# Kernel optimization log

Hardware: AMD Instinct MI355X
Metric: run time of the kernel (lower is better)

## Reference

```python
import jax, jax.numpy as jnp
import numpy as np

N2, N1, N0 = 16000, 4000, 1000   # leaf / mid / target node counts
DEG = 32                          # sampled neighbors per target
IN_DIM, OUT_DIM, H = 256, 64, 4
NEG = -9e15
ALPHA = 0.2                       # LeakyReLU slope


def setup_inputs() -> dict:
    key = jax.random.key(0)
    ks = jax.random.split(key, 10)
    s = 0.05  # xavier-ish scale
    x = jax.random.normal(ks[0], (N2, IN_DIM), jnp.float32)
    W0 = jax.random.normal(ks[1], (H, IN_DIM, OUT_DIM), jnp.float32) * s
    a0 = jax.random.normal(ks[2], (H, 2 * OUT_DIM), jnp.float32) * s
    W1 = jax.random.normal(ks[3], (H, OUT_DIM * H, OUT_DIM), jnp.float32) * s
    a1 = jax.random.normal(ks[4], (H, 2 * OUT_DIM), jnp.float32) * s
    lin_W = jax.random.normal(ks[5], (OUT_DIM * H, OUT_DIM * H), jnp.float32) * s
    lin_b = jax.random.normal(ks[6], (OUT_DIM * H,), jnp.float32) * s
    # level-1 edges: n1 targets, each with DEG sampled leaf neighbors + self-loop
    adj1_tgt = jnp.concatenate([jnp.repeat(jnp.arange(N1), DEG), jnp.arange(N1)]).astype(jnp.int32)
    adj1_nbr = jnp.concatenate([jax.random.randint(ks[7], (N1 * DEG,), 0, N2),
                                jnp.arange(N1)]).astype(jnp.int32)
    # level-0 edges: n0 targets, each with DEG sampled mid neighbors + self-loop
    adj0_tgt = jnp.concatenate([jnp.repeat(jnp.arange(N0), DEG), jnp.arange(N0)]).astype(jnp.int32)
    adj0_nbr = jnp.concatenate([jax.random.randint(ks[8], (N0 * DEG,), 0, N1),
                                jnp.arange(N0)]).astype(jnp.int32)
    return {"x": x, "W0": W0, "a0": a0, "W1": W1, "a1": a1,
            "lin_W": lin_W, "lin_b": lin_b,
            "adj1_tgt": adj1_tgt, "adj1_nbr": adj1_nbr,
            "adj0_tgt": adj0_tgt, "adj0_nbr": adj0_nbr,
            "n0": N0, "n1": N1}


def _att_layer(x, W, a, tgt, nbr, T):
    # x: [N, D], W: [H, D, O], a: [H, 2O]; multi-head GAT layer (eval mode, no dropout)
    h = jnp.einsum('nd,hdo->hno', x, W)                      # [H, N, O]
    O = h.shape[-1]
    e = jax.nn.leaky_relu(
        jnp.einsum('heo,ho->he', h[:, tgt], a[:, :O]) +
        jnp.einsum('heo,ho->he', h[:, nbr], a[:, O:]), ALPHA)  # [H, E]
    N = h.shape[1]
    att = jnp.full((h.shape[0], T, N), NEG, x.dtype).at[:, tgt, nbr].set(e)
    att = jax.nn.softmax(att, axis=-1)                        # dense edge-softmax
    hp = jax.nn.elu(jnp.einsum('htn,hno->hto', att, h))       # [H, T, O]
    return jnp.transpose(hp, (1, 0, 2)).reshape(T, -1)        # cat heads -> [T, H*O]


def reference(x, W0, a0, W1, a1, lin_W, lin_b,
              adj1_tgt, adj1_nbr, adj0_tgt, adj0_nbr, n0, n1):
    x1 = _att_layer(x, W0, a0, adj1_tgt, adj1_nbr, n1)   # [n1, H*O]
    x2 = _att_layer(x1, W1, a1, adj0_tgt, adj0_nbr, n0)  # [n0, H*O]
    return jnp.tanh(x2 @ lin_W.T + lin_b)                # Linear + Tanh
```

## Files before the change

### kernel.cpp

```cpp
#include <hip/hip_runtime.h>
#include <math.h>

#define N2C 16000
#define N1C 4000
#define N0C 1000
#define DEG 32
#define CH 256
#define NHEAD 4
#define ODIM 64
#define ALPHA 0.2f
#define LDP 264

typedef __attribute__((ext_vector_type(8))) short bf16x8;
typedef __attribute__((ext_vector_type(4))) float f32x4;

__device__ __forceinline__ ushort f2bf(float f) {
    unsigned u = __float_as_uint(f);
    unsigned r = (u + 0x7fffu + ((u >> 16) & 1u)) >> 16;
    return (ushort)r;
}
__device__ __forceinline__ float bf2f(ushort h) {
    return __uint_as_float(((unsigned)h) << 16);
}

__global__ __launch_bounds__(256) void repack_kernel(
    const float* __restrict__ W0, const float* __restrict__ W1,
    const float* __restrict__ linW,
    ushort* __restrict__ Wth, ushort* __restrict__ Wtl)
{
    int g = blockIdx.x * 256 + threadIdx.x;
    int mat = g >> 16;
    int idx = g & 65535;
    int c = idx >> 8, k = idx & 255;
    float v;
    if (mat == 0)      v = W0[(c >> 6) * (256 * 64) + k * 64 + (c & 63)];
    else if (mat == 1) v = W1[(c >> 6) * (256 * 64) + k * 64 + (c & 63)];
    else               v = linW[c * 256 + k];
    ushort h = f2bf(v);
    Wth[g] = h;
    Wtl[g] = f2bf(v - bf2f(h));
}

template<int RT, int EPI, int AF32, int SC>
__global__ __launch_bounds__(256) void gemm_mfma(
    const float* __restrict__ Af,
    const ushort* __restrict__ Ah, const ushort* __restrict__ Al,
    const ushort* __restrict__ Bh, const ushort* __restrict__ Bl,
    const float* __restrict__ bias, const float* __restrict__ avec,
    float* __restrict__ out, float* __restrict__ s_t, float* __restrict__ s_n, int M)
{
    __shared__ ushort sah[AF32 ? RT * 16 * LDP : 1];
    __shared__ ushort sal[AF32 ? RT * 16 * LDP : 1];

    const int wave = threadIdx.x >> 6;
    const int lane = threadIdx.x & 63;
    const int quad = lane >> 4, l16 = lane & 15;
    const int row0 = blockIdx.x * (RT * 16);
    const int col0 = wave * 64;

    if (AF32) {
        for (int idx = threadIdx.x; idx < RT * 16 * 64; idx += 256) {
            int row = idx >> 6, c4 = idx & 63;
            int gr = row0 + row; if (gr >= M) gr = M - 1;
            float4 f = ((const float4*)Af)[gr * 64 + c4];
            ushort4 h, l;
            h.x = f2bf(f.x); l.x = f2bf(f.x - bf2f(h.x));
            h.y = f2bf(f.y); l.y = f2bf(f.y - bf2f(h.y));
            h.z = f2bf(f.z); l.z = f2bf(f.z - bf2f(h.z));
            h.w = f2bf(f.w); l.w = f2bf(f.w - bf2f(h.w));
            *(ushort4*)(&sah[row * LDP + c4 * 4]) = h;
            *(ushort4*)(&sal[row * LDP + c4 * 4]) = l;
        }
        __syncthreads();
    }

    f32x4 acc[RT][4];
#pragma unroll
    for (int r = 0; r < RT; ++r)
#pragma unroll
        for (int c = 0; c < 4; ++c) acc[r][c] = (f32x4){0.f, 0.f, 0.f, 0.f};

    int arow[RT];
#pragma unroll
    for (int r = 0; r < RT; ++r) {
        int rr = row0 + r * 16 + l16;
        arow[r] = (rr < M) ? rr : (M - 1);
    }
    const int kbase = quad * 8;

    for (int k0 = 0; k0 < 256; k0 += 32) {
        bf16x8 a_h[RT], a_l[RT], b_h[4], b_l[4];
#pragma unroll
        for (int r = 0; r < RT; ++r) {
            if (AF32) {
                int loff = (r * 16 + l16) * LDP + k0 + kbase;
                a_h[r] = *(const bf16x8*)(&sah[loff]);
                a_l[r] = *(const bf16x8*)(&sal[loff]);
            } else {
                int off = arow[r] * 256 + k0 + kbase;
                a_h[r] = *(const bf16x8*)(Ah + off);
                a_l[r] = *(const bf16x8*)(Al + off);
            }
        }
#pragma unroll
        for (int c = 0; c < 4; ++c) {
            int off = (col0 + c * 16 + l16) * 256 + k0 + kbase;
            b_h[c] = *(const bf16x8*)(Bh + off);
            b_l[c] = *(const bf16x8*)(Bl + off);
        }
#pragma unroll
        for (int r = 0; r < RT; ++r)
#pragma unroll
            for (int c = 0; c < 4; ++c) {
                acc[r][c] = __builtin_amdgcn_mfma_f32_16x16x32_bf16(a_h[r], b_h[c], acc[r][c], 0, 0, 0);
                acc[r][c] = __builtin_amdgcn_mfma_f32_16x16x32_bf16(a_h[r], b_l[c], acc[r][c], 0, 0, 0);
                acc[r][c] = __builtin_amdgcn_mfma_f32_16x16x32_bf16(a_l[r], b_h[c], acc[r][c], 0, 0, 0);
            }
    }

#pragma unroll
    for (int r = 0; r < RT; ++r)
#pragma unroll
        for (int c = 0; c < 4; ++c) {
            int col = col0 + c * 16 + l16;
#pragma unroll
            for (int reg = 0; reg < 4; ++reg) {
                int row = row0 + r * 16 + quad * 4 + reg;
                if (row < M) {
                    float v = acc[r][c][reg];
                    if (EPI == 1) v = tanhf(v + bias[col]);
                    out[row * 256 + col] = v;
                }
            }
        }

    if (SC) {
        float at[4], an[4];
#pragma unroll
        for (int c = 0; c < 4; ++c) {
            at[c] = avec[wave * 128 + c * 16 + l16];
            an[c] = avec[wave * 128 + 64 + c * 16 + l16];
        }
#pragma unroll
        for (int r = 0; r < RT; ++r) {
            float pt[4] = {0.f, 0.f, 0.f, 0.f}, pn[4] = {0.f, 0.f, 0.f, 0.f};
#pragma unroll
            for (int c = 0; c < 4; ++c)
#pragma unroll
                for (int reg = 0; reg < 4; ++reg) {
                    pt[reg] += acc[r][c][reg] * at[c];
                    pn[reg] += acc[r][c][reg] * an[c];
                }
#pragma unroll
            for (int reg = 0; reg < 4; ++reg)
#pragma unroll
                for (int m = 1; m < 16; m <<= 1) {
                    pt[reg] += __shfl_xor(pt[reg], m);
                    pn[reg] += __shfl_xor(pn[reg], m);
                }
            if (l16 == 0) {
#pragma unroll
                for (int reg = 0; reg < 4; ++reg) {
                    int row = row0 + r * 16 + quad * 4 + reg;
                    if (row < M) {
                        s_t[wave * M + row] = pt[reg];
                        s_n[wave * M + row] = pn[reg];
                    }
                }
            }
        }
    }
}

__global__ __launch_bounds__(256) void att_kernel(
    const float* __restrict__ hprev, const int* __restrict__ nbr_arr,
    const float* __restrict__ s_t, const float* __restrict__ s_n,
    ushort* __restrict__ outhi, ushort* __restrict__ outlo, int T, int Nsrc)
{
    __shared__ int nbr[DEG + 1];
    __shared__ float att_s[NHEAD][DEG + 3];
    __shared__ float4 red[4][64];
    const int tgt = blockIdx.x;
    const int t = threadIdx.x;
    const int lane = t & 63;
    if (t < DEG) nbr[t] = nbr_arr[tgt * DEG + t];
    else if (t == DEG) nbr[DEG] = nbr_arr[T * DEG + tgt];
    __syncthreads();

    {
        const int hd = t >> 6;
        int me = (lane <= DEG) ? nbr[lane] : -1;
        int k = (lane <= DEG) ? 1 : 0;
#pragma unroll
        for (int j = 0; j < DEG; ++j) {
            int v = __shfl(me, j);
            if (j < lane && v == me) k = 0;
        }
        float e = s_t[hd * Nsrc + tgt] + ((lane <= DEG) ? s_n[hd * Nsrc + me] : 0.f);
        e = (e >= 0.f) ? e : ALPHA * e;
        float em = k ? e : -1e30f;
        float m = em;
#pragma unroll
        for (int off = 1; off < 64; off <<= 1) m = fmaxf(m, __shfl_xor(m, off));
        float w = k ? __expf(e - m) : 0.f;
        float Z = w;
#pragma unroll
        for (int off = 1; off < 64; off <<= 1) Z += __shfl_xor(Z, off);
        if (lane <= DEG) att_s[hd][lane] = w / Z;
    }
    __syncthreads();

    const int cq = t & 63;
    const int rg = t >> 6;
    const int hd = cq >> 4;
    const float4* hp4 = (const float4*)hprev;
    float4 acc = make_float4(0.f, 0.f, 0.f, 0.f);
#pragma unroll
    for (int ii = 0; ii < 9; ++ii) {
        int i = rg + ii * 4;
        if (i <= DEG) {
            float w = att_s[hd][i];
            float4 v = hp4[(size_t)nbr[i] * 64 + cq];
            acc.x += w * v.x; acc.y += w * v.y;
            acc.z += w * v.z; acc.w += w * v.w;
        }
    }
    red[rg][cq] = acc;
    __syncthreads();
    if (t < 64) {
        float4 s0 = red[0][t], s1 = red[1][t], s2 = red[2][t], s3 = red[3][t];
        float4 s;
        s.x = s0.x + s1.x + s2.x + s3.x;
        s.y = s0.y + s1.y + s2.y + s3.y;
        s.z = s0.z + s1.z + s2.z + s3.z;
        s.w = s0.w + s1.w + s2.w + s3.w;
        s.x = (s.x > 0.f) ? s.x : expm1f(s.x);
        s.y = (s.y > 0.f) ? s.y : expm1f(s.y);
        s.z = (s.z > 0.f) ? s.z : expm1f(s.z);
        s.w = (s.w > 0.f) ? s.w : expm1f(s.w);
        ushort4 h, l;
        h.x = f2bf(s.x); l.x = f2bf(s.x - bf2f(h.x));
        h.y = f2bf(s.y); l.y = f2bf(s.y - bf2f(h.y));
        h.z = f2bf(s.z); l.z = f2bf(s.z - bf2f(h.z));
        h.w = f2bf(s.w); l.w = f2bf(s.w - bf2f(h.w));
        ((ushort4*)outhi)[tgt * 64 + t] = h;
        ((ushort4*)outlo)[tgt * 64 + t] = l;
    }
}

extern "C" void kernel_launch(void* const* d_in, const int* in_sizes, int n_in,
                              void* d_out, int out_size, void* d_ws, size_t ws_size,
                              hipStream_t stream)
{
    const float* x    = (const float*)d_in[0];
    const float* W0   = (const float*)d_in[1];
    const float* a0   = (const float*)d_in[2];
    const float* W1   = (const float*)d_in[3];
    const float* a1   = (const float*)d_in[4];
    const float* linW = (const float*)d_in[5];
    const float* linb = (const float*)d_in[6];
    const int* adj1_nbr = (const int*)d_in[8];
    const int* adj0_nbr = (const int*)d_in[10];

    char* base = (char*)d_ws;
    ushort* Wth = (ushort*)base;
    ushort* Wtl = Wth + 3 * 65536;
    float*  st  = (float*)(base + 786432);
    float*  sn  = st + 65536;
    float*  h0  = (float*)(base + 1310720);
    ushort* xhi = (ushort*)(base + 1310720 + 16384000);
    ushort* xlo = xhi + 4096000;

    repack_kernel<<<768, 256, 0, stream>>>(W0, W1, linW, Wth, Wtl);

    gemm_mfma<2, 0, 1, 1><<<N2C / 32, 256, 0, stream>>>(
        x, nullptr, nullptr, Wth, Wtl, nullptr, a0, h0, st, sn, N2C);
    att_kernel<<<N1C, 256, 0, stream>>>(h0, adj1_nbr, st, sn, xhi, xlo, N1C, N2C);

    gemm_mfma<1, 0, 0, 1><<<N1C / 16, 256, 0, stream>>>(
        nullptr, xhi, xlo, Wth + 65536, Wtl + 65536, nullptr, a1, h0, st, sn, N1C);
    att_kernel<<<N0C, 256, 0, stream>>>(h0, adj0_nbr, st, sn, xhi, xlo, N0C, N1C);

    gemm_mfma<1, 1, 0, 0><<<(N0C + 15) / 16, 256, 0, stream>>>(
        nullptr, xhi, xlo, Wth + 131072, Wtl + 131072, linb, nullptr,
        (float*)d_out, nullptr, nullptr, N0C);
}
```

Measured before the change: 166.8 us.

## Fuse attention aggregation into the following GEMM via shared-memory staging

Attention softmax and neighbor aggregation now run inside the next layer's GEMM kernel. Each block computes 16 target rows, one per wave per iteration, and writes the split bf16 hi/lo results into shared memory. The GEMM tile then reads A from LDS instead of global memory. This removes two kernel launches and the global round-trip of the intermediate bf16 activations, but the aggregation kernels drop from 4000/1000 blocks to 250/63, so less parallelism is available for the gather-bound part.

```diff
diff --git a/kernel.cpp b/kernel.cpp
--- a/kernel.cpp
+++ b/kernel.cpp
@@ -5,9 +5,7 @@
 #define N1C 4000
 #define N0C 1000
 #define DEG 32
-#define CH 256
 #define NHEAD 4
-#define ODIM 64
 #define ALPHA 0.2f
 #define LDP 264
 
@@ -41,24 +39,21 @@
     Wtl[g] = f2bf(v - bf2f(h));
 }
 
-template<int RT, int EPI, int AF32, int SC>
-__global__ __launch_bounds__(256) void gemm_mfma(
+template<int RT, int EPI, int AMODE, int SC>
+__device__ __forceinline__ void gemm_tile(
+    int row0, int M,
     const float* __restrict__ Af,
-    const ushort* __restrict__ Ah, const ushort* __restrict__ Al,
     const ushort* __restrict__ Bh, const ushort* __restrict__ Bl,
     const float* __restrict__ bias, const float* __restrict__ avec,
-    float* __restrict__ out, float* __restrict__ s_t, float* __restrict__ s_n, int M)
-{
-    __shared__ ushort sah[AF32 ? RT * 16 * LDP : 1];
-    __shared__ ushort sal[AF32 ? RT * 16 * LDP : 1];
-
+    float* __restrict__ out, float* __restrict__ s_t, float* __restrict__ s_n,
+    ushort* sah, ushort* sal)
+{
     const int wave = threadIdx.x >> 6;
     const int lane = threadIdx.x & 63;
     const int quad = lane >> 4, l16 = lane & 15;
-    const int row0 = blockIdx.x * (RT * 16);
     const int col0 = wave * 64;
 
-    if (AF32) {
+    if (AMODE == 1) {
         for (int idx = threadIdx.x; idx < RT * 16 * 64; idx += 256) {
             int row = idx >> 6, c4 = idx & 63;
             int gr = row0 + row; if (gr >= M) gr = M - 1;
@@ -80,27 +75,14 @@
 #pragma unroll
         for (int c = 0; c < 4; ++c) acc[r][c] = (f32x4){0.f, 0.f, 0.f, 0.f};
 
-    int arow[RT];
-#pragma unroll
-    for (int r = 0; r < RT; ++r) {
-        int rr = row0 + r * 16 + l16;
-        arow[r] = (rr < M) ? rr : (M - 1);
-    }
     const int kbase = quad * 8;
-
     for (int k0 = 0; k0 < 256; k0 += 32) {
         bf16x8 a_h[RT], a_l[RT], b_h[4], b_l[4];
 #pragma unroll
         for (int r = 0; r < RT; ++r) {
-            if (AF32) {
-                int loff = (r * 16 + l16) * LDP + k0 + kbase;
-                a_h[r] = *(const bf16x8*)(&sah[loff]);
-                a_l[r] = *(const bf16x8*)(&sal[loff]);
-            } else {
-                int off = arow[r] * 256 + k0 + kbase;
-                a_h[r] = *(const bf16x8*)(Ah + off);
-                a_l[r] = *(const bf16x8*)(Al + off);
-            }
+            int loff = (r * 16 + l16) * LDP + k0 + kbase;
+            a_h[r] = *(const bf16x8*)(&sah[loff]);
+            a_l[r] = *(const bf16x8*)(&sal[loff]);
         }
 #pragma unroll
         for (int c = 0; c < 4; ++c) {
@@ -172,80 +154,93 @@
     }
 }
 
-__global__ __launch_bounds__(256) void att_kernel(
+__global__ __launch_bounds__(256) void gemm1_kernel(
+    const float* __restrict__ x, const float* __restrict__ a0,
+    const ushort* __restrict__ Bh, const ushort* __restrict__ Bl,
+    float* __restrict__ h0, float* __restrict__ s_t, float* __restrict__ s_n)
+{
+    __shared__ ushort sah[32 * LDP];
+    __shared__ ushort sal[32 * LDP];
+    gemm_tile<2, 0, 1, 1>(blockIdx.x * 32, N2C, x, Bh, Bl, nullptr, a0,
+                          h0, s_t, s_n, sah, sal);
+}
+
+template<int EPI, int SC>
+__global__ __launch_bounds__(256) void ag_kernel(
     const float* __restrict__ hprev, const int* __restrict__ nbr_arr,
-    const float* __restrict__ s_t, const float* __restrict__ s_n,
-    ushort* __restrict__ outhi, ushort* __restrict__ outlo, int T, int Nsrc)
-{
-    __shared__ int nbr[DEG + 1];
-    __shared__ float att_s[NHEAD][DEG + 3];
-    __shared__ float4 red[4][64];
-    const int tgt = blockIdx.x;
-    const int t = threadIdx.x;
-    const int lane = t & 63;
-    if (t < DEG) nbr[t] = nbr_arr[tgt * DEG + t];
-    else if (t == DEG) nbr[DEG] = nbr_arr[T * DEG + tgt];
+    const float* __restrict__ s_tin, const float* __restrict__ s_nin,
+    const ushort* __restrict__ Bh, const ushort* __restrict__ Bl,
+    const float* __restrict__ bias, const float* __restrict__ avec,
+    float* __restrict__ out, float* __restrict__ s_tout, float* __restrict__ s_nout,
+    int T, int Nsrc)
+{
+    __shared__ ushort sah[16 * LDP];
+    __shared__ ushort sal[16 * LDP];
+    __shared__ float wts[4][NHEAD][DEG + 2];
+
+    const int wave = threadIdx.x >> 6;
+    const int lane = threadIdx.x & 63;
+    const int row0 = blockIdx.x * 16;
+    const float4* hp4 = (const float4*)hprev;
+
+#pragma unroll
+    for (int r = 0; r < 4; ++r) {
+        const int tg = r * 4 + wave;
+        const int tgt = row0 + tg;
+        if (tgt < T) {
+            int me = 0;
+            if (lane < DEG) me = nbr_arr[tgt * DEG + lane];
+            else if (lane == DEG) me = nbr_arr[T * DEG + tgt];
+            int k = (lane <= DEG) ? 1 : 0;
+#pragma unroll
+            for (int j = 0; j < DEG; ++j) {
+                int v = __shfl(me, j);
+                if (j < lane && v == me) k = 0;
+            }
+#pragma unroll
+            for (int hd = 0; hd < NHEAD; ++hd) {
+                float e = s_tin[hd * Nsrc + tgt] + s_nin[hd * Nsrc + me];
+                e = (e >= 0.f) ? e : ALPHA * e;
+                float em = k ? e : -1e30f;
+                float m = em;
+#pragma unroll
+                for (int off = 1; off < 64; off <<= 1) m = fmaxf(m, __shfl_xor(m, off));
+                float w = k ? __expf(e - m) : 0.f;
+                float Z = w;
+#pragma unroll
+                for (int off = 1; off < 64; off <<= 1) Z += __shfl_xor(Z, off);
+                if (lane <= DEG) wts[wave][hd][lane] = w / Z;
+            }
+            const int hd = lane >> 4;
+            float4 acc = make_float4(0.f, 0.f, 0.f, 0.f);
+#pragma unroll
+            for (int e = 0; e <= DEG; ++e) {
+                int row = __shfl(me, e);
+                float wt = wts[wave][hd][e];
+                float4 v = hp4[(size_t)row * 64 + lane];
+                acc.x += wt * v.x; acc.y += wt * v.y;
+                acc.z += wt * v.z; acc.w += wt * v.w;
+            }
+            acc.x = (acc.x > 0.f) ? acc.x : expm1f(acc.x);
+            acc.y = (acc.y > 0.f) ? acc.y : expm1f(acc.y);
+            acc.z = (acc.z > 0.f) ? acc.z : expm1f(acc.z);
+            acc.w = (acc.w > 0.f) ? acc.w : expm1f(acc.w);
+            ushort4 h, l;
+            h.x = f2bf(acc.x); l.x = f2bf(acc.x - bf2f(h.x));
+            h.y = f2bf(acc.y); l.y = f2bf(acc.y - bf2f(h.y));
+            h.z = f2bf(acc.z); l.z = f2bf(acc.z - bf2f(h.z));
+            h.w = f2bf(acc.w); l.w = f2bf(acc.w - bf2f(h.w));
+            *(ushort4*)(&sah[tg * LDP + lane * 4]) = h;
+            *(ushort4*)(&sal[tg * LDP + lane * 4]) = l;
+        } else {
+            ushort4 z = make_ushort4(0, 0, 0, 0);
+            *(ushort4*)(&sah[tg * LDP + lane * 4]) = z;
+            *(ushort4*)(&sal[tg * LDP + lane * 4]) = z;
+        }
+    }
     __syncthreads();
-
-    {
-        const int hd = t >> 6;
-        int me = (lane <= DEG) ? nbr[lane] : -1;
-        int k = (lane <= DEG) ? 1 : 0;
-#pragma unroll
-        for (int j = 0; j < DEG; ++j) {
-            int v = __shfl(me, j);
-            if (j < lane && v == me) k = 0;
-        }
-        float e = s_t[hd * Nsrc + tgt] + ((lane <= DEG) ? s_n[hd * Nsrc + me] : 0.f);
-        e = (e >= 0.f) ? e : ALPHA * e;
-        float em = k ? e : -1e30f;
-        float m = em;
-#pragma unroll
-        for (int off = 1; off < 64; off <<= 1) m = fmaxf(m, __shfl_xor(m, off));
-        float w = k ? __expf(e - m) : 0.f;
-        float Z = w;
-#pragma unroll
-        for (int off = 1; off < 64; off <<= 1) Z += __shfl_xor(Z, off);
-        if (lane <= DEG) att_s[hd][lane] = w / Z;
-    }
-    __syncthreads();
-
-    const int cq = t & 63;
-    const int rg = t >> 6;
-    const int hd = cq >> 4;
-    const float4* hp4 = (const float4*)hprev;
-    float4 acc = make_float4(0.f, 0.f, 0.f, 0.f);
-#pragma unroll
-    for (int ii = 0; ii < 9; ++ii) {
-        int i = rg + ii * 4;
-        if (i <= DEG) {
-            float w = att_s[hd][i];
-            float4 v = hp4[(size_t)nbr[i] * 64 + cq];
-            acc.x += w * v.x; acc.y += w * v.y;
-            acc.z += w * v.z; acc.w += w * v.w;
-        }
-    }
-    red[rg][cq] = acc;
-    __syncthreads();
-    if (t < 64) {
-        float4 s0 = red[0][t], s1 = red[1][t], s2 = red[2][t], s3 = red[3][t];
-        float4 s;
-        s.x = s0.x + s1.x + s2.x + s3.x;
-        s.y = s0.y + s1.y + s2.y + s3.y;
-        s.z = s0.z + s1.z + s2.z + s3.z;
-        s.w = s0.w + s1.w + s2.w + s3.w;
-        s.x = (s.x > 0.f) ? s.x : expm1f(s.x);
-        s.y = (s.y > 0.f) ? s.y : expm1f(s.y);
-        s.z = (s.z > 0.f) ? s.z : expm1f(s.z);
-        s.w = (s.w > 0.f) ? s.w : expm1f(s.w);
-        ushort4 h, l;
-        h.x = f2bf(s.x); l.x = f2bf(s.x - bf2f(h.x));
-        h.y = f2bf(s.y); l.y = f2bf(s.y - bf2f(h.y));
-        h.z = f2bf(s.z); l.z = f2bf(s.z - bf2f(h.z));
-        h.w = f2bf(s.w); l.w = f2bf(s.w - bf2f(h.w));
-        ((ushort4*)outhi)[tgt * 64 + t] = h;
-        ((ushort4*)outlo)[tgt * 64 + t] = l;
-    }
+    gemm_tile<1, EPI, 2, SC>(row0, T, nullptr, Bh, Bl, bias, avec,
+                             out, s_tout, s_nout, sah, sal);
 }
 
 extern "C" void kernel_launch(void* const* d_in, const int* in_sizes, int n_in,
@@ -261,27 +256,26 @@
     const float* linb = (const float*)d_in[6];
     const int* adj1_nbr = (const int*)d_in[8];
     const int* adj0_nbr = (const int*)d_in[10];
-
-    char* base = (char*)d_ws;
-    ushort* Wth = (ushort*)base;
-    ushort* Wtl = Wth + 3 * 65536;
-    float*  st  = (float*)(base + 786432);
-    float*  sn  = st + 65536;
-    float*  h0  = (float*)(base + 1310720);
-    ushort* xhi = (ushort*)(base + 1310720 + 16384000);
-    ushort* xlo = xhi + 4096000;
+    char* ws = (char*)d_ws;
+
+    ushort* Wth = (ushort*)ws;
+    ushort* Wtl = (ushort*)(ws + 393216);
+    float*  st0 = (float*)(ws + 786432);
+    float*  sn0 = (float*)(ws + 1048576);
+    float*  st1 = (float*)(ws + 1310720);
+    float*  sn1 = (float*)(ws + 1376256);
+    float*  h0  = (float*)(ws + 1441792);
+    float*  h1  = (float*)(ws + 17825792);
 
     repack_kernel<<<768, 256, 0, stream>>>(W0, W1, linW, Wth, Wtl);
 
-    gemm_mfma<2, 0, 1, 1><<<N2C / 32, 256, 0, stream>>>(
-        x, nullptr, nullptr, Wth, Wtl, nullptr, a0, h0, st, sn, N2C);
-    att_kernel<<<N1C, 256, 0, stream>>>(h0, adj1_nbr, st, sn, xhi, xlo, N1C, N2C);
-
-    gemm_mfma<1, 0, 0, 1><<<N1C / 16, 256, 0, stream>>>(
-        nullptr, xhi, xlo, Wth + 65536, Wtl + 65536, nullptr, a1, h0, st, sn, N1C);
-    att_kernel<<<N0C, 256, 0, stream>>>(h0, adj0_nbr, st, sn, xhi, xlo, N0C, N1C);
-
-    gemm_mfma<1, 1, 0, 0><<<(N0C + 15) / 16, 256, 0, stream>>>(
-        nullptr, xhi, xlo, Wth + 131072, Wtl + 131072, linb, nullptr,
-        (float*)d_out, nullptr, nullptr, N0C);
-}
+    gemm1_kernel<<<N2C / 32, 256, 0, stream>>>(x, a0, Wth, Wtl, h0, st0, sn0);
+
+    ag_kernel<0, 1><<<N1C / 16, 256, 0, stream>>>(
+        h0, adj1_nbr, st0, sn0, Wth + 65536, Wtl + 65536, nullptr, a1,
+        h1, st1, sn1, N1C, N2C);
+
+    ag_kernel<1, 0><<<(N0C + 15) / 16, 256, 0, stream>>>(
+        h1, adj0_nbr, st1, sn1, Wth + 131072, Wtl + 131072, linb, nullptr,
+        (float*)d_out, nullptr, nullptr, N0C, N1C);
+}
```

Result: slower. 186.5 us (+11.8%).
